# Optimization experiments

Measured on AMD Instinct MI355X. Metric: run time of the kernel, lower is better.

Reference implementation:

```python
import jax, jax.numpy as jnp
import numpy as np
from jax import lax

D_MODEL = 64      # feature_dim
D_STATE = 16      # state_dim
D_CONV = 4        # conv_dim
EXPAND = 2
D_INNER = EXPAND * D_MODEL          # 128
DT_RANK = (D_MODEL + 15) // 16      # ceil(d_model/16) = 4, mamba default
IN_DIM = 64
LN_EPS = 1e-3                        # keras LayerNormalization default epsilon


def setup_inputs() -> dict:
    key = jax.random.key(0)
    ks = jax.random.split(key, 12)
    B, L = 16, 8192
    s = 0.02
    x = jax.random.normal(ks[0], (B, L, IN_DIM), jnp.float32)
    W_in = jax.random.normal(ks[1], (IN_DIM, D_MODEL), jnp.float32) * s
    b_in = jnp.zeros((D_MODEL,), jnp.float32)
    in_proj_w = jax.random.normal(ks[2], (D_MODEL, 2 * D_INNER), jnp.float32) * s
    conv_w = jax.random.normal(ks[3], (D_INNER, D_CONV), jnp.float32) * 0.1
    conv_b = jnp.zeros((D_INNER,), jnp.float32)
    x_proj_w = jax.random.normal(ks[4], (D_INNER, DT_RANK + 2 * D_STATE), jnp.float32) * s
    dt_proj_w = jax.random.normal(ks[5], (DT_RANK, D_INNER), jnp.float32) * (DT_RANK ** -0.5)
    # dt bias init so softplus(dt) lands roughly in [dt_min, dt_max]
    dt = jnp.exp(jax.random.uniform(ks[6], (D_INNER,)) * (np.log(0.1) - np.log(0.001)) + np.log(0.001))
    dt_proj_b = dt + jnp.log(-jnp.expm1(-dt))  # inverse softplus
    A_log = jnp.log(jnp.broadcast_to(jnp.arange(1, D_STATE + 1, dtype=jnp.float32), (D_INNER, D_STATE)))
    D_skip = jnp.ones((D_INNER,), jnp.float32)
    out_proj_w = jax.random.normal(ks[7], (D_INNER, D_MODEL), jnp.float32) * s
    ln_gamma = jnp.ones((D_MODEL,), jnp.float32)
    ln_beta = jnp.zeros((D_MODEL,), jnp.float32)
    return {"x": x, "W_in": W_in, "b_in": b_in, "in_proj_w": in_proj_w,
            "conv_w": conv_w, "conv_b": conv_b, "x_proj_w": x_proj_w,
            "dt_proj_w": dt_proj_w, "dt_proj_b": dt_proj_b, "A_log": A_log,
            "D_skip": D_skip, "out_proj_w": out_proj_w,
            "ln_gamma": ln_gamma, "ln_beta": ln_beta}


def reference(x, W_in, b_in, in_proj_w, conv_w, conv_b, x_proj_w,
              dt_proj_w, dt_proj_b, A_log, D_skip, out_proj_w, ln_gamma, ln_beta):
    B, L, _ = x.shape
    # Conv1D kernel_size=1 input projection
    xin = x @ W_in + b_in                          # [B,L,D_MODEL]
    # --- Mamba ---
    xz = xin @ in_proj_w                           # [B,L,2*D_INNER]
    xc, z = xz[..., :D_INNER], xz[..., D_INNER:]
    # causal depthwise conv (groups=d_inner, padding=d_conv-1, crop to L)
    xp = jnp.pad(xc, ((0, 0), (D_CONV - 1, 0), (0, 0)))
    xconv = conv_b
    for k in range(D_CONV):
        xconv = xconv + xp[:, k:k + L, :] * conv_w[:, k]
    u = jax.nn.silu(xconv)                         # [B,L,D_INNER]
    dbc = u @ x_proj_w                             # [B,L,DT_RANK+2*D_STATE]
    dt = jax.nn.softplus(dbc[..., :DT_RANK] @ dt_proj_w + dt_proj_b)   # [B,L,D_INNER]
    Bm = dbc[..., DT_RANK:DT_RANK + D_STATE]       # [B,L,D_STATE]
    Cm = dbc[..., DT_RANK + D_STATE:]              # [B,L,D_STATE]
    A = -jnp.exp(A_log)                            # [D_INNER,D_STATE]

    def step(h, xs):
        dt_t, b_t, c_t, u_t = xs                   # [B,Di],[B,Ds],[B,Ds],[B,Di]
        dA = jnp.exp(dt_t[:, :, None] * A)         # [B,Di,Ds]
        h = dA * h + (dt_t * u_t)[:, :, None] * b_t[:, None, :]
        y = jnp.einsum('bds,bs->bd', h, c_t)
        return h, y

    xs = (jnp.swapaxes(dt, 0, 1), jnp.swapaxes(Bm, 0, 1),
          jnp.swapaxes(Cm, 0, 1), jnp.swapaxes(u, 0, 1))
    h0 = jnp.zeros((B, D_INNER, D_STATE), x.dtype)
    _, ys = lax.scan(step, h0, xs)                 # ys: [L,B,D_INNER]
    y = jnp.swapaxes(ys, 0, 1) + u * D_skip
    y = y * jax.nn.silu(z)
    h_out = y @ out_proj_w                         # [B,L,D_MODEL]
    # residual + LayerNorm
    res = h_out + xin
    mu = jnp.mean(res, axis=-1, keepdims=True)
    var = jnp.mean(jnp.square(res - mu), axis=-1, keepdims=True)
    return ln_gamma * (res - mu) * lax.rsqrt(var + LN_EPS) + ln_beta
```

## Files before the change

kernel.cpp:

```cpp
#include <hip/hip_runtime.h>
#include <hip/hip_bf16.h>

#define B_SZ   16
#define L_SZ   8192
#define DM     64
#define DI     128
#define NCH    128
#define CLEN   64
#define CH     64
#define RT     80
#define PA     72
#define PU     136
#define PC     132
#define LN_EPS 1e-3f

typedef float  f4 __attribute__((ext_vector_type(4)));
typedef short  s8 __attribute__((ext_vector_type(8)));
typedef unsigned short u16;
typedef unsigned int   u32;
#define MFMA16 __builtin_amdgcn_mfma_f32_16x16x32_bf16

__device__ __forceinline__ u16 f2bfu(float f) {
    u32 u = __float_as_uint(f);
    return (u16)((u + 0x7FFFu + ((u >> 16) & 1u)) >> 16);
}
__device__ __forceinline__ u32 pk2bf(float a, float b) {
    return (u32)f2bfu(a) | ((u32)f2bfu(b) << 16);
}
__device__ __forceinline__ float bflo(u32 u) { return __uint_as_float(u << 16); }
__device__ __forceinline__ float bfhi(u32 u) { return __uint_as_float(u & 0xFFFF0000u); }
__device__ __forceinline__ float bfu2f(u16 h) { return __uint_as_float((u32)h << 16); }
__device__ __forceinline__ float fsig(float v) {
    return __builtin_amdgcn_rcpf(1.f + __expf(-v));
}
__device__ __forceinline__ float fsp(float v) {
    return fmaxf(v, 0.f) + __logf(1.f + __expf(-fabsf(v)));
}

__global__ __launch_bounds__(256) void k_prep(
    const float* __restrict__ W_in, const float* __restrict__ in_proj,
    const float* __restrict__ x_proj, const float* __restrict__ Wout,
    u16* __restrict__ Wf1, u16* __restrict__ Wf2,
    u16* __restrict__ Wf3, u16* __restrict__ Wf4)
{
    const int tid = threadIdx.x;
    for (int g = tid; g < 512; g += 256) {
        int lane = g & 63, ks = (g >> 6) & 1, nt = g >> 7;
        int n = nt * 16 + (lane & 15), kb = ks * 32 + (lane >> 4) * 8;
        for (int j = 0; j < 8; j++) Wf1[g * 8 + j] = f2bfu(W_in[(kb + j) * 64 + n]);
    }
    for (int g = tid; g < 2048; g += 256) {
        int lane = g & 63, ks = (g >> 6) & 1, nt = g >> 7;
        int n = nt * 16 + (lane & 15), kb = ks * 32 + (lane >> 4) * 8;
        for (int j = 0; j < 8; j++) Wf2[g * 8 + j] = f2bfu(in_proj[(kb + j) * 256 + n]);
    }
    for (int g = tid; g < 768; g += 256) {
        int lane = g & 63, ks = (g >> 6) & 3, nt = g >> 8;
        int n = nt * 16 + (lane & 15), kb = ks * 32 + (lane >> 4) * 8;
        for (int j = 0; j < 8; j++)
            Wf3[g * 8 + j] = f2bfu(n < 36 ? x_proj[(kb + j) * 36 + n] : 0.f);
    }
    for (int g = tid; g < 1024; g += 256) {
        int lane = g & 63, ks = (g >> 6) & 3, nt = g >> 8;
        int n = nt * 16 + (lane & 15), kb = ks * 32 + (lane >> 4) * 8;
        for (int j = 0; j < 8; j++) Wf4[g * 8 + j] = f2bfu(Wout[(kb + j) * 64 + n]);
    }
}

__global__ __launch_bounds__(256) void k_frontend(
    const float* __restrict__ x, const float* __restrict__ b_in,
    const float* __restrict__ conv_w, const float* __restrict__ conv_b,
    const float* __restrict__ dt_w, const float* __restrict__ dt_b,
    const u16* __restrict__ Wf1, const u16* __restrict__ Wf2, const u16* __restrict__ Wf3,
    float* __restrict__ xin_g, u16* __restrict__ u_g, float* __restrict__ dt_g,
    float* __restrict__ B_g, float* __restrict__ C_g, u16* __restrict__ sz_g)
{
    __shared__ __align__(16) char sm[41088];
    u16*   smA   = (u16*)sm;
    u16*   smB   = (u16*)(sm + 11520);
    u16*   smU   = (u16*)sm;
    float* smDtr = (float*)(sm + 17408);
    u16*   smC   = (u16*)(sm + 23040);

    const int tid = threadIdx.x;
    const int w = tid >> 6, lane = tid & 63;
    const int n16 = lane & 15, quad = lane >> 4;
    const int b = blockIdx.y, c0 = blockIdx.x * CH;
    const long long tokbase = (long long)b * L_SZ + c0;

    for (int idx = tid; idx < RT * 16; idx += 256) {
        int r = idx >> 4, c4 = idx & 15;
        int l = c0 - 3 + r;
        float4 v = make_float4(0.f, 0.f, 0.f, 0.f);
        if (r < 67 && l >= 0)
            v = *(const float4*)(x + ((long long)b * L_SZ + l) * 64 + c4 * 4);
        *(uint2*)((char*)smA + r * 144 + c4 * 8) = make_uint2(pk2bf(v.x, v.y), pk2bf(v.z, v.w));
    }
    __syncthreads();

    {
        s8 b0 = *(const s8*)(Wf1 + ((w * 2 + 0) * 64 + lane) * 8);
        s8 b1 = *(const s8*)(Wf1 + ((w * 2 + 1) * 64 + lane) * 8);
        float bias = b_in[w * 16 + n16];
        for (int m = 0; m < 5; m++) {
            int ar = m * 16 + n16;
            s8 a0 = *(const s8*)(smA + ar * PA + quad * 8);
            s8 a1 = *(const s8*)(smA + ar * PA + 32 + quad * 8);
            f4 acc = {0.f, 0.f, 0.f, 0.f};
            acc = MFMA16(a0, b0, acc, 0, 0, 0);
            acc = MFMA16(a1, b1, acc, 0, 0, 0);
#pragma unroll
            for (int reg = 0; reg < 4; reg++) {
                int rr = m * 16 + quad * 4 + reg;
                float v = acc[reg] + bias;
                smB[rr * PA + w * 16 + n16] = f2bfu(v);
                if (rr >= 3 && rr < 67)
                    xin_g[(tokbase + rr - 3) * 64 + w * 16 + n16] = v;
            }
        }
    }
    __syncthreads();

    {
        s8 bf[4][2];
#pragma unroll
        for (int i = 0; i < 4; i++)
#pragma unroll
            for (int ks = 0; ks < 2; ks++)
                bf[i][ks] = *(const s8*)(Wf2 + (((w * 4 + i) * 2 + ks) * 64 + lane) * 8);
        for (int m = 0; m < 5; m++) {
            int ar = m * 16 + n16;
            s8 a0 = *(const s8*)(smB + ar * PA + quad * 8);
            s8 a1 = *(const s8*)(smB + ar * PA + 32 + quad * 8);
#pragma unroll
            for (int i = 0; i < 4; i++) {
                f4 acc = {0.f, 0.f, 0.f, 0.f};
                acc = MFMA16(a0, bf[i][0], acc, 0, 0, 0);
                acc = MFMA16(a1, bf[i][1], acc, 0, 0, 0);
                int cg = (w * 4 + i) * 16 + n16;
#pragma unroll
                for (int reg = 0; reg < 4; reg++) {
                    int rr = m * 16 + quad * 4 + reg;
                    float v = acc[reg];
                    if (cg < 128) {
                        if (rr < 67) {
                            int l = c0 - 3 + rr;
                            smC[rr * PC + cg] = f2bfu(l >= 0 ? v : 0.f);
                        }
                    } else if (rr >= 3 && rr < 67) {
                        sz_g[(tokbase + rr - 3) * 128 + (cg - 128)] = f2bfu(v * fsig(v));
                    }
                }
            }
        }
    }
    __syncthreads();

    {
        const int d2 = lane * 2, ctb = w * 16;
        float4 cw0 = ((const float4*)conv_w)[d2];
        float4 cw1 = ((const float4*)conv_w)[d2 + 1];
        float cb0 = conv_b[d2], cb1 = conv_b[d2 + 1];
        u32 r0 = *(const u32*)((char*)smC + (ctb + 0) * 264 + lane * 4);
        u32 r1 = *(const u32*)((char*)smC + (ctb + 1) * 264 + lane * 4);
        u32 r2 = *(const u32*)((char*)smC + (ctb + 2) * 264 + lane * 4);
#pragma unroll 4
        for (int j = 0; j < 16; j++) {
            int ct = ctb + j;
            u32 r3 = *(const u32*)((char*)smC + (ct + 3) * 264 + lane * 4);
            float v0 = cb0 + bflo(r0) * cw0.x + bflo(r1) * cw0.y + bflo(r2) * cw0.z + bflo(r3) * cw0.w;
            float v1 = cb1 + bfhi(r0) * cw1.x + bfhi(r1) * cw1.y + bfhi(r2) * cw1.z + bfhi(r3) * cw1.w;
            u32 pk = pk2bf(v0 * fsig(v0), v1 * fsig(v1));
            *(u32*)(u_g + (tokbase + ct) * 128 + d2) = pk;
            *(u32*)(smU + ct * PU + d2) = pk;
            r0 = r1; r1 = r2; r2 = r3;
        }
    }
    __syncthreads();

    {
        s8 bf3[3][4];
#pragma unroll
        for (int nt = 0; nt < 3; nt++)
#pragma unroll
            for (int ks = 0; ks < 4; ks++)
                bf3[nt][ks] = *(const s8*)(Wf3 + ((nt * 4 + ks) * 64 + lane) * 8);
        f4 acc[3] = {{0.f,0.f,0.f,0.f},{0.f,0.f,0.f,0.f},{0.f,0.f,0.f,0.f}};
        int ar = w * 16 + n16;
#pragma unroll
        for (int ks = 0; ks < 4; ks++) {
            s8 a = *(const s8*)(smU + ar * PU + ks * 32 + quad * 8);
#pragma unroll
            for (int nt = 0; nt < 3; nt++) acc[nt] = MFMA16(a, bf3[nt][ks], acc[nt], 0, 0, 0);
        }
#pragma unroll
        for (int nt = 0; nt < 3; nt++) {
            int c = nt * 16 + n16;
#pragma unroll
            for (int reg = 0; reg < 4; reg++) {
                int rr = w * 16 + quad * 4 + reg;
                float v = acc[nt][reg];
                long long t = tokbase + rr;
                if (c < 4)       smDtr[rr * 4 + c] = v;
                else if (c < 20) B_g[t * 16 + (c - 4)] = v;
                else if (c < 36) C_g[t * 16 + (c - 20)] = v;
            }
        }
    }
    __syncthreads();

    {
        const int o2 = lane * 2, grp = w;
        float w00 = dt_w[o2],       w01 = dt_w[o2 + 1];
        float w10 = dt_w[128 + o2], w11 = dt_w[128 + o2 + 1];
        float w20 = dt_w[256 + o2], w21 = dt_w[256 + o2 + 1];
        float w30 = dt_w[384 + o2], w31 = dt_w[384 + o2 + 1];
        float b0 = dt_b[o2], b1 = dt_b[o2 + 1];
#pragma unroll 4
        for (int j = 0; j < 16; j++) {
            int ct = grp * 16 + j;
            float4 q = *(const float4*)(smDtr + ct * 4);
            float v0 = b0 + q.x * w00 + q.y * w10 + q.z * w20 + q.w * w30;
            float v1 = b1 + q.x * w01 + q.y * w11 + q.z * w21 + q.w * w31;
            *(float2*)(dt_g + (tokbase + ct) * 128 + o2) = make_float2(fsp(v0), fsp(v1));
        }
    }
}

__global__ __launch_bounds__(128) void k_scan1(
    const float* __restrict__ dt_g, const u16* __restrict__ u_g,
    const float* __restrict__ B_g, const float* __restrict__ A_log,
    float* __restrict__ hl_ws, float* __restrict__ sdt_ws)
{
    const int d = threadIdx.x, c = blockIdx.x, b = blockIdx.y;
    float A[16];
#pragma unroll
    for (int s = 0; s < 16; s++) A[s] = -__expf(A_log[d * 16 + s]);
    const float A0 = A[0];
    bool chain = true;
#pragma unroll
    for (int s = 1; s < 16; s++)
        chain = chain && (fabsf(A[s] - (float)(s + 1) * A0) <= 1e-4f * fabsf(A[s]));

    float h[16];
#pragma unroll
    for (int s = 0; s < 16; s++) h[s] = 0.f;
    float sdt = 0.f;
    const long long tok0 = (long long)b * L_SZ + (long long)c * CLEN;

    if (chain) {
        for (int i = 0; i < CLEN; i++) {
            const long long t = tok0 + i;
            float dtv = dt_g[t * 128 + d];
            float uv  = bfu2f(u_g[t * 128 + d]);
            const float4* Bp = (const float4*)(B_g + t * 16);
            float4 B0 = Bp[0], B1 = Bp[1], B2 = Bp[2], B3 = Bp[3];
            float Bv[16] = { B0.x, B0.y, B0.z, B0.w, B1.x, B1.y, B1.z, B1.w,
                             B2.x, B2.y, B2.z, B2.w, B3.x, B3.y, B3.z, B3.w };
            float du = dtv * uv;  sdt += dtv;
            float p = __expf(dtv * A0), dA = p;
            h[0] = dA * h[0] + du * Bv[0];
#pragma unroll
            for (int s = 1; s < 16; s++) { dA *= p; h[s] = dA * h[s] + du * Bv[s]; }
        }
    } else {
        for (int i = 0; i < CLEN; i++) {
            const long long t = tok0 + i;
            float dtv = dt_g[t * 128 + d];
            float uv  = bfu2f(u_g[t * 128 + d]);
            const float4* Bp = (const float4*)(B_g + t * 16);
            float4 B0 = Bp[0], B1 = Bp[1], B2 = Bp[2], B3 = Bp[3];
            float Bv[16] = { B0.x, B0.y, B0.z, B0.w, B1.x, B1.y, B1.z, B1.w,
                             B2.x, B2.y, B2.z, B2.w, B3.x, B3.y, B3.z, B3.w };
            float du = dtv * uv;  sdt += dtv;
#pragma unroll
            for (int s = 0; s < 16; s++) h[s] = __expf(dtv * A[s]) * h[s] + du * Bv[s];
        }
    }

    float4* hp4 = (float4*)(hl_ws + (((long long)b * NCH + c) * 128 + d) * 16);
    hp4[0] = make_float4(h[0], h[1], h[2], h[3]);
    hp4[1] = make_float4(h[4], h[5], h[6], h[7]);
    hp4[2] = make_float4(h[8], h[9], h[10], h[11]);
    hp4[3] = make_float4(h[12], h[13], h[14], h[15]);
    sdt_ws[((long long)b * NCH + c) * 128 + d] = sdt;
}

__global__ __launch_bounds__(256) void k_combine(
    const float* __restrict__ A_log, const float* __restrict__ hl_ws,
    const float* __restrict__ sdt_ws, float* __restrict__ hin_ws)
{
    int gid = blockIdx.x * 256 + threadIdx.x;
    int b = gid >> 11;
    int rem = gid & 2047;
    int d = rem >> 4;
    float A = -__expf(A_log[rem]);
    float h = 0.f;
    for (int c = 0; c < NCH; c++) {
        long long o = ((long long)b * NCH + c) * 2048 + rem;
        hin_ws[o] = h;
        float sdt = sdt_ws[((long long)b * NCH + c) * 128 + d];
        h = __expf(A * sdt) * h + hl_ws[o];
    }
}

__global__ __launch_bounds__(128) void k_scan3(
    const float* __restrict__ dt_g, const u16* __restrict__ u_g,
    const float* __restrict__ B_g, const float* __restrict__ C_g,
    const u16* __restrict__ sz_g, const float* __restrict__ A_log,
    const float* __restrict__ D_skip, const float* __restrict__ hin_ws,
    u16* __restrict__ y_g)
{
    const int d = threadIdx.x, c = blockIdx.x, b = blockIdx.y;
    float A[16];
#pragma unroll
    for (int s = 0; s < 16; s++) A[s] = -__expf(A_log[d * 16 + s]);
    const float A0 = A[0];
    bool chain = true;
#pragma unroll
    for (int s = 1; s < 16; s++)
        chain = chain && (fabsf(A[s] - (float)(s + 1) * A0) <= 1e-4f * fabsf(A[s]));

    float h[16];
    {
        const float4* hp = (const float4*)(hin_ws + (((long long)b * NCH + c) * 128 + d) * 16);
        float4 h0 = hp[0], h1 = hp[1], h2 = hp[2], h3 = hp[3];
        h[0]=h0.x; h[1]=h0.y; h[2]=h0.z; h[3]=h0.w;
        h[4]=h1.x; h[5]=h1.y; h[6]=h1.z; h[7]=h1.w;
        h[8]=h2.x; h[9]=h2.y; h[10]=h2.z; h[11]=h2.w;
        h[12]=h3.x; h[13]=h3.y; h[14]=h3.z; h[15]=h3.w;
    }
    const float Dv = D_skip[d];
    const long long tok0 = (long long)b * L_SZ + (long long)c * CLEN;

    if (chain) {
        for (int i = 0; i < CLEN; i++) {
            const long long t = tok0 + i;
            float dtv = dt_g[t * 128 + d];
            float uv  = bfu2f(u_g[t * 128 + d]);
            const float4* Bp = (const float4*)(B_g + t * 16);
            float4 B0 = Bp[0], B1 = Bp[1], B2 = Bp[2], B3 = Bp[3];
            float Bv[16] = { B0.x, B0.y, B0.z, B0.w, B1.x, B1.y, B1.z, B1.w,
                             B2.x, B2.y, B2.z, B2.w, B3.x, B3.y, B3.z, B3.w };
            const float4* Cp = (const float4*)(C_g + t * 16);
            float4 C0 = Cp[0], C1 = Cp[1], C2 = Cp[2], C3 = Cp[3];
            float Cv[16] = { C0.x, C0.y, C0.z, C0.w, C1.x, C1.y, C1.z, C1.w,
                             C2.x, C2.y, C2.z, C2.w, C3.x, C3.y, C3.z, C3.w };
            float du = dtv * uv;
            float p = __expf(dtv * A0), dA = p;
            h[0] = dA * h[0] + du * Bv[0];
            float ysum = h[0] * Cv[0];
#pragma unroll
            for (int s = 1; s < 16; s++) {
                dA *= p;
                h[s] = dA * h[s] + du * Bv[s];
                ysum += h[s] * Cv[s];
            }
            float szv = bfu2f(sz_g[t * 128 + d]);
            y_g[t * 128 + d] = f2bfu((ysum + uv * Dv) * szv);
        }
    } else {
        for (int i = 0; i < CLEN; i++) {
            const long long t = tok0 + i;
            float dtv = dt_g[t * 128 + d];
            float uv  = bfu2f(u_g[t * 128 + d]);
            const float4* Bp = (const float4*)(B_g + t * 16);
            float4 B0 = Bp[0], B1 = Bp[1], B2 = Bp[2], B3 = Bp[3];
            float Bv[16] = { B0.x, B0.y, B0.z, B0.w, B1.x, B1.y, B1.z, B1.w,
                             B2.x, B2.y, B2.z, B2.w, B3.x, B3.y, B3.z, B3.w };
            const float4* Cp = (const float4*)(C_g + t * 16);
            float4 C0 = Cp[0], C1 = Cp[1], C2 = Cp[2], C3 = Cp[3];
            float Cv[16] = { C0.x, C0.y, C0.z, C0.w, C1.x, C1.y, C1.z, C1.w,
                             C2.x, C2.y, C2.z, C2.w, C3.x, C3.y, C3.z, C3.w };
            float du = dtv * uv;
            float ysum = 0.f;
#pragma unroll
            for (int s = 0; s < 16; s++) {
                h[s] = __expf(dtv * A[s]) * h[s] + du * Bv[s];
                ysum += h[s] * Cv[s];
            }
            float szv = bfu2f(sz_g[t * 128 + d]);
            y_g[t * 128 + d] = f2bfu((ysum + uv * Dv) * szv);
        }
    }
}

__global__ __launch_bounds__(256) void k_epilogue(
    const u16* __restrict__ y_g, const float* __restrict__ xin_g,
    const u16* __restrict__ Wf4, const float* __restrict__ gamma,
    const float* __restrict__ beta, float* __restrict__ out)
{
    __shared__ __align__(16) char sm[34048];
    u16*   yA  = (u16*)sm;
    float* smR = (float*)(sm + 17408);

    const int tid = threadIdx.x;
    const int w = tid >> 6, lane = tid & 63;
    const int n16 = lane & 15, quad = lane >> 4;
    const long long t0 = (long long)blockIdx.x * 64;

    for (int idx = tid; idx < 64 * 64; idx += 256) {
        int r = idx >> 6, cp = idx & 63;
        u32 v = ((const u32*)y_g)[(t0 + r) * 64 + cp];
        *(u32*)((char*)yA + r * 272 + cp * 4) = v;
    }
    __syncthreads();

    {
        s8 bf[4];
#pragma unroll
        for (int ks = 0; ks < 4; ks++)
            bf[ks] = *(const s8*)(Wf4 + ((w * 4 + ks) * 64 + lane) * 8);
#pragma unroll
        for (int m = 0; m < 4; m++) {
            int ar = m * 16 + n16;
            f4 acc = {0.f, 0.f, 0.f, 0.f};
#pragma unroll
            for (int ks = 0; ks < 4; ks++) {
                s8 a = *(const s8*)(yA + ar * PU + ks * 32 + quad * 8);
                acc = MFMA16(a, bf[ks], acc, 0, 0, 0);
            }
#pragma unroll
            for (int reg = 0; reg < 4; reg++) {
                int rr = m * 16 + quad * 4 + reg;
                smR[rr * 65 + w * 16 + n16] = acc[reg];
            }
        }
    }
    __syncthreads();

    {
        int o = tid & 63, wv = tid >> 6;
        float g = gamma[o], bb = beta[o];
        for (int j = 0; j < 16; j++) {
            int rr = wv * 16 + j;
            float r = smR[rr * 65 + o] + xin_g[(t0 + rr) * 64 + o];
            float s = r;
#pragma unroll
            for (int mS = 0; mS < 6; mS++) s += __shfl_xor(s, 1 << mS, 64);
            float mu = s * (1.f / 64.f);
            float dv = r - mu;
            float vs = dv * dv;
#pragma unroll
            for (int mS = 0; mS < 6; mS++) vs += __shfl_xor(vs, 1 << mS, 64);
            out[(t0 + rr) * 64 + o] = g * dv * rsqrtf(vs * (1.f / 64.f) + LN_EPS) + bb;
        }
    }
}

extern "C" void kernel_launch(void* const* d_in, const int* in_sizes, int n_in,
                              void* d_out, int out_size, void* d_ws, size_t ws_size,
                              hipStream_t stream)
{
    const float* x       = (const float*)d_in[0];
    const float* W_in    = (const float*)d_in[1];
    const float* b_in    = (const float*)d_in[2];
    const float* in_proj = (const float*)d_in[3];
    const float* conv_w  = (const float*)d_in[4];
    const float* conv_b  = (const float*)d_in[5];
    const float* x_proj  = (const float*)d_in[6];
    const float* dt_w    = (const float*)d_in[7];
    const float* dt_b    = (const float*)d_in[8];
    const float* A_log   = (const float*)d_in[9];
    const float* D_skip  = (const float*)d_in[10];
    const float* Wout    = (const float*)d_in[11];
    const float* gamma   = (const float*)d_in[12];
    const float* beta    = (const float*)d_in[13];
    float* out = (float*)d_out;

    const long long NT = (long long)B_SZ * L_SZ;
    char* ws = (char*)d_ws;
    float*  xin_g = (float*)ws;   ws += NT * 64 * 4;
    float*  dt_g  = (float*)ws;   ws += NT * 128 * 4;
    float*  B_g   = (float*)ws;   ws += NT * 16 * 4;
    float*  C_g   = (float*)ws;   ws += NT * 16 * 4;
    u16*    u_g   = (u16*)ws;     ws += NT * 128 * 2;
    u16*    sz_g  = (u16*)ws;     ws += NT * 128 * 2;
    u16*    y_g   = (u16*)ws;     ws += NT * 128 * 2;
    float*  hl_ws  = (float*)ws;  ws += (long long)B_SZ * NCH * 2048 * 4;
    float*  sdt_ws = (float*)ws;  ws += (long long)B_SZ * NCH * 128 * 4;
    float*  hin_ws = (float*)ws;  ws += (long long)B_SZ * NCH * 2048 * 4;
    u16* Wf1 = (u16*)ws; ws += 4096 * 2;
    u16* Wf2 = (u16*)ws; ws += 16384 * 2;
    u16* Wf3 = (u16*)ws; ws += 6144 * 2;
    u16* Wf4 = (u16*)ws; ws += 8192 * 2;

    k_prep<<<1, 256, 0, stream>>>(W_in, in_proj, x_proj, Wout, Wf1, Wf2, Wf3, Wf4);

    k_frontend<<<dim3(L_SZ / CH, B_SZ), 256, 0, stream>>>(
        x, b_in, conv_w, conv_b, dt_w, dt_b, Wf1, Wf2, Wf3,
        xin_g, u_g, dt_g, B_g, C_g, sz_g);

    k_scan1<<<dim3(NCH, B_SZ), 128, 0, stream>>>(
        dt_g, u_g, B_g, A_log, hl_ws, sdt_ws);

    k_combine<<<128, 256, 0, stream>>>(A_log, hl_ws, sdt_ws, hin_ws);

    k_scan3<<<dim3(NCH, B_SZ), 128, 0, stream>>>(
        dt_g, u_g, B_g, C_g, sz_g, A_log, D_skip, hin_ws, y_g);

    k_epilogue<<<2048, 256, 0, stream>>>(y_g, xin_g, Wf4, gamma, beta, out);
}
```

Measured before the change: 310.4 us.

## Fuse chunk-local scan into frontend and fuse output scan with epilogue

The first chunked scan pass moves into the frontend kernel and reads dt inputs, u and B from shared memory, recomputing dt from the low-rank projection, with state split across two thread halves. The second scan pass is merged with the out-projection and LayerNorm epilogue, so y stays in shared memory and the y_g round trip and two launches go away. In exchange, only half the threads do scan work in the fused output kernel, the frontend gains more shared memory and a serial tail, and occupancy may drop.

```diff
diff --git a/kernel.cpp b/kernel.cpp
--- a/kernel.cpp
+++ b/kernel.cpp
@@ -71,16 +71,19 @@
     const float* __restrict__ x, const float* __restrict__ b_in,
     const float* __restrict__ conv_w, const float* __restrict__ conv_b,
     const float* __restrict__ dt_w, const float* __restrict__ dt_b,
+    const float* __restrict__ A_log,
     const u16* __restrict__ Wf1, const u16* __restrict__ Wf2, const u16* __restrict__ Wf3,
     float* __restrict__ xin_g, u16* __restrict__ u_g, float* __restrict__ dt_g,
-    float* __restrict__ B_g, float* __restrict__ C_g, u16* __restrict__ sz_g)
+    float* __restrict__ B_g, float* __restrict__ C_g, u16* __restrict__ sz_g,
+    float* __restrict__ hl_ws, float* __restrict__ sdt_ws)
 {
-    __shared__ __align__(16) char sm[41088];
+    __shared__ __align__(16) char sm[45184];
     u16*   smA   = (u16*)sm;
     u16*   smB   = (u16*)(sm + 11520);
     u16*   smU   = (u16*)sm;
     float* smDtr = (float*)(sm + 17408);
     u16*   smC   = (u16*)(sm + 23040);
+    float* smBB  = (float*)(sm + 41088);
 
     const int tid = threadIdx.x;
     const int w = tid >> 6, lane = tid & 63;
@@ -202,7 +205,7 @@
                 float v = acc[nt][reg];
                 long long t = tokbase + rr;
                 if (c < 4)       smDtr[rr * 4 + c] = v;
-                else if (c < 20) B_g[t * 16 + (c - 4)] = v;
+                else if (c < 20) { B_g[t * 16 + (c - 4)] = v; smBB[rr * 16 + (c - 4)] = v; }
                 else if (c < 36) C_g[t * 16 + (c - 20)] = v;
             }
         }
@@ -225,65 +228,61 @@
             *(float2*)(dt_g + (tokbase + ct) * 128 + o2) = make_float2(fsp(v0), fsp(v1));
         }
     }
-}
-
-__global__ __launch_bounds__(128) void k_scan1(
-    const float* __restrict__ dt_g, const u16* __restrict__ u_g,
-    const float* __restrict__ B_g, const float* __restrict__ A_log,
-    float* __restrict__ hl_ws, float* __restrict__ sdt_ws)
-{
-    const int d = threadIdx.x, c = blockIdx.x, b = blockIdx.y;
-    float A[16];
-#pragma unroll
-    for (int s = 0; s < 16; s++) A[s] = -__expf(A_log[d * 16 + s]);
-    const float A0 = A[0];
-    bool chain = true;
-#pragma unroll
-    for (int s = 1; s < 16; s++)
-        chain = chain && (fabsf(A[s] - (float)(s + 1) * A0) <= 1e-4f * fabsf(A[s]));
-
-    float h[16];
-#pragma unroll
-    for (int s = 0; s < 16; s++) h[s] = 0.f;
-    float sdt = 0.f;
-    const long long tok0 = (long long)b * L_SZ + (long long)c * CLEN;
-
-    if (chain) {
-        for (int i = 0; i < CLEN; i++) {
-            const long long t = tok0 + i;
-            float dtv = dt_g[t * 128 + d];
-            float uv  = bfu2f(u_g[t * 128 + d]);
-            const float4* Bp = (const float4*)(B_g + t * 16);
-            float4 B0 = Bp[0], B1 = Bp[1], B2 = Bp[2], B3 = Bp[3];
-            float Bv[16] = { B0.x, B0.y, B0.z, B0.w, B1.x, B1.y, B1.z, B1.w,
-                             B2.x, B2.y, B2.z, B2.w, B3.x, B3.y, B3.z, B3.w };
-            float du = dtv * uv;  sdt += dtv;
-            float p = __expf(dtv * A0), dA = p;
-            h[0] = dA * h[0] + du * Bv[0];
-#pragma unroll
-            for (int s = 1; s < 16; s++) { dA *= p; h[s] = dA * h[s] + du * Bv[s]; }
-        }
-    } else {
-        for (int i = 0; i < CLEN; i++) {
-            const long long t = tok0 + i;
-            float dtv = dt_g[t * 128 + d];
-            float uv  = bfu2f(u_g[t * 128 + d]);
-            const float4* Bp = (const float4*)(B_g + t * 16);
-            float4 B0 = Bp[0], B1 = Bp[1], B2 = Bp[2], B3 = Bp[3];
-            float Bv[16] = { B0.x, B0.y, B0.z, B0.w, B1.x, B1.y, B1.z, B1.w,
-                             B2.x, B2.y, B2.z, B2.w, B3.x, B3.y, B3.z, B3.w };
-            float du = dtv * uv;  sdt += dtv;
-#pragma unroll
-            for (int s = 0; s < 16; s++) h[s] = __expf(dtv * A[s]) * h[s] + du * Bv[s];
-        }
-    }
-
-    float4* hp4 = (float4*)(hl_ws + (((long long)b * NCH + c) * 128 + d) * 16);
-    hp4[0] = make_float4(h[0], h[1], h[2], h[3]);
-    hp4[1] = make_float4(h[4], h[5], h[6], h[7]);
-    hp4[2] = make_float4(h[8], h[9], h[10], h[11]);
-    hp4[3] = make_float4(h[12], h[13], h[14], h[15]);
-    sdt_ws[((long long)b * NCH + c) * 128 + d] = sdt;
+
+    {
+        const int d = tid & 127, oct = tid >> 7;
+        const float bw0 = dt_w[d], bw1 = dt_w[128 + d], bw2 = dt_w[256 + d], bw3 = dt_w[384 + d];
+        const float bdt = dt_b[d];
+        const float A0 = -__expf(A_log[d * 16]);
+        float Aq[8];
+#pragma unroll
+        for (int k = 0; k < 8; k++) Aq[k] = -__expf(A_log[d * 16 + oct * 8 + k]);
+        bool chain = true;
+#pragma unroll
+        for (int k = 0; k < 8; k++)
+            chain = chain && (fabsf(Aq[k] - (float)(oct * 8 + k + 1) * A0) <= 1e-4f * fabsf(Aq[k]));
+
+        float h[8];
+#pragma unroll
+        for (int k = 0; k < 8; k++) h[k] = 0.f;
+        float sdt = 0.f;
+
+        if (chain) {
+            for (int i = 0; i < CH; i++) {
+                float4 q = *(const float4*)(smDtr + i * 4);
+                float dtv = fsp(bdt + q.x * bw0 + q.y * bw1 + q.z * bw2 + q.w * bw3);
+                float uv = bfu2f(smU[i * PU + d]);
+                float du = dtv * uv;  sdt += dtv;
+                float4 b0 = *(const float4*)(smBB + i * 16 + oct * 8);
+                float4 b1 = *(const float4*)(smBB + i * 16 + oct * 8 + 4);
+                float Bv[8] = {b0.x, b0.y, b0.z, b0.w, b1.x, b1.y, b1.z, b1.w};
+                float p = __expf(dtv * A0);
+                float dA;
+                if (oct == 0) dA = p;
+                else { float p2 = p * p, p4 = p2 * p2, p8 = p4 * p4; dA = p8 * p; }
+                h[0] = dA * h[0] + du * Bv[0];
+#pragma unroll
+                for (int k = 1; k < 8; k++) { dA *= p; h[k] = dA * h[k] + du * Bv[k]; }
+            }
+        } else {
+            for (int i = 0; i < CH; i++) {
+                float4 q = *(const float4*)(smDtr + i * 4);
+                float dtv = fsp(bdt + q.x * bw0 + q.y * bw1 + q.z * bw2 + q.w * bw3);
+                float uv = bfu2f(smU[i * PU + d]);
+                float du = dtv * uv;  sdt += dtv;
+                float4 b0 = *(const float4*)(smBB + i * 16 + oct * 8);
+                float4 b1 = *(const float4*)(smBB + i * 16 + oct * 8 + 4);
+                float Bv[8] = {b0.x, b0.y, b0.z, b0.w, b1.x, b1.y, b1.z, b1.w};
+#pragma unroll
+                for (int k = 0; k < 8; k++) h[k] = __expf(dtv * Aq[k]) * h[k] + du * Bv[k];
+            }
+        }
+        float4* hp = (float4*)(hl_ws + (((long long)b * NCH + blockIdx.x) * 128 + d) * 16 + oct * 8);
+        hp[0] = make_float4(h[0], h[1], h[2], h[3]);
+        hp[1] = make_float4(h[4], h[5], h[6], h[7]);
+        if (oct == 0)
+            sdt_ws[((long long)b * NCH + blockIdx.x) * 128 + d] = sdt;
+    }
 }
 
 __global__ __launch_bounds__(256) void k_combine(
@@ -304,108 +303,101 @@
     }
 }
 
-__global__ __launch_bounds__(128) void k_scan3(
+__global__ __launch_bounds__(256) void k_scan3f(
     const float* __restrict__ dt_g, const u16* __restrict__ u_g,
     const float* __restrict__ B_g, const float* __restrict__ C_g,
     const u16* __restrict__ sz_g, const float* __restrict__ A_log,
     const float* __restrict__ D_skip, const float* __restrict__ hin_ws,
-    u16* __restrict__ y_g)
+    const u16* __restrict__ Wf4, const float* __restrict__ xin_g,
+    const float* __restrict__ gamma, const float* __restrict__ beta,
+    float* __restrict__ out)
 {
-    const int d = threadIdx.x, c = blockIdx.x, b = blockIdx.y;
-    float A[16];
-#pragma unroll
-    for (int s = 0; s < 16; s++) A[s] = -__expf(A_log[d * 16 + s]);
-    const float A0 = A[0];
-    bool chain = true;
-#pragma unroll
-    for (int s = 1; s < 16; s++)
-        chain = chain && (fabsf(A[s] - (float)(s + 1) * A0) <= 1e-4f * fabsf(A[s]));
-
-    float h[16];
-    {
-        const float4* hp = (const float4*)(hin_ws + (((long long)b * NCH + c) * 128 + d) * 16);
-        float4 h0 = hp[0], h1 = hp[1], h2 = hp[2], h3 = hp[3];
-        h[0]=h0.x; h[1]=h0.y; h[2]=h0.z; h[3]=h0.w;
-        h[4]=h1.x; h[5]=h1.y; h[6]=h1.z; h[7]=h1.w;
-        h[8]=h2.x; h[9]=h2.y; h[10]=h2.z; h[11]=h2.w;
-        h[12]=h3.x; h[13]=h3.y; h[14]=h3.z; h[15]=h3.w;
-    }
-    const float Dv = D_skip[d];
-    const long long tok0 = (long long)b * L_SZ + (long long)c * CLEN;
-
-    if (chain) {
-        for (int i = 0; i < CLEN; i++) {
-            const long long t = tok0 + i;
-            float dtv = dt_g[t * 128 + d];
-            float uv  = bfu2f(u_g[t * 128 + d]);
-            const float4* Bp = (const float4*)(B_g + t * 16);
-            float4 B0 = Bp[0], B1 = Bp[1], B2 = Bp[2], B3 = Bp[3];
-            float Bv[16] = { B0.x, B0.y, B0.z, B0.w, B1.x, B1.y, B1.z, B1.w,
-                             B2.x, B2.y, B2.z, B2.w, B3.x, B3.y, B3.z, B3.w };
-            const float4* Cp = (const float4*)(C_g + t * 16);
-            float4 C0 = Cp[0], C1 = Cp[1], C2 = Cp[2], C3 = Cp[3];
-            float Cv[16] = { C0.x, C0.y, C0.z, C0.w, C1.x, C1.y, C1.z, C1.w,
-                             C2.x, C2.y, C2.z, C2.w, C3.x, C3.y, C3.z, C3.w };
-            float du = dtv * uv;
-            float p = __expf(dtv * A0), dA = p;
-            h[0] = dA * h[0] + du * Bv[0];
-            float ysum = h[0] * Cv[0];
-#pragma unroll
-            for (int s = 1; s < 16; s++) {
-                dA *= p;
-                h[s] = dA * h[s] + du * Bv[s];
-                ysum += h[s] * Cv[s];
-            }
-            float szv = bfu2f(sz_g[t * 128 + d]);
-            y_g[t * 128 + d] = f2bfu((ysum + uv * Dv) * szv);
-        }
-    } else {
-        for (int i = 0; i < CLEN; i++) {
-            const long long t = tok0 + i;
-            float dtv = dt_g[t * 128 + d];
-            float uv  = bfu2f(u_g[t * 128 + d]);
-            const float4* Bp = (const float4*)(B_g + t * 16);
-            float4 B0 = Bp[0], B1 = Bp[1], B2 = Bp[2], B3 = Bp[3];
-            float Bv[16] = { B0.x, B0.y, B0.z, B0.w, B1.x, B1.y, B1.z, B1.w,
-                             B2.x, B2.y, B2.z, B2.w, B3.x, B3.y, B3.z, B3.w };
-            const float4* Cp = (const float4*)(C_g + t * 16);
-            float4 C0 = Cp[0], C1 = Cp[1], C2 = Cp[2], C3 = Cp[3];
-            float Cv[16] = { C0.x, C0.y, C0.z, C0.w, C1.x, C1.y, C1.z, C1.w,
-                             C2.x, C2.y, C2.z, C2.w, C3.x, C3.y, C3.z, C3.w };
-            float du = dtv * uv;
-            float ysum = 0.f;
-#pragma unroll
-            for (int s = 0; s < 16; s++) {
-                h[s] = __expf(dtv * A[s]) * h[s] + du * Bv[s];
-                ysum += h[s] * Cv[s];
-            }
-            float szv = bfu2f(sz_g[t * 128 + d]);
-            y_g[t * 128 + d] = f2bfu((ysum + uv * Dv) * szv);
-        }
-    }
-}
-
-__global__ __launch_bounds__(256) void k_epilogue(
-    const u16* __restrict__ y_g, const float* __restrict__ xin_g,
-    const u16* __restrict__ Wf4, const float* __restrict__ gamma,
-    const float* __restrict__ beta, float* __restrict__ out)
-{
-    __shared__ __align__(16) char sm[34048];
-    u16*   yA  = (u16*)sm;
-    float* smR = (float*)(sm + 17408);
+    __shared__ __align__(16) char sm[17408];
+    u16*   smY = (u16*)sm;
+    float* smR = (float*)sm;
 
     const int tid = threadIdx.x;
+    const int c = blockIdx.x, b = blockIdx.y;
+    const long long t0 = (long long)b * L_SZ + (long long)c * CLEN;
+
+    if (tid < 128) {
+        const int d = tid;
+        float A[16];
+#pragma unroll
+        for (int s = 0; s < 16; s++) A[s] = -__expf(A_log[d * 16 + s]);
+        const float A0 = A[0];
+        bool chain = true;
+#pragma unroll
+        for (int s = 1; s < 16; s++)
+            chain = chain && (fabsf(A[s] - (float)(s + 1) * A0) <= 1e-4f * fabsf(A[s]));
+
+        float h[16];
+        {
+            const float4* hp = (const float4*)(hin_ws + (((long long)b * NCH + c) * 128 + d) * 16);
+            float4 h0 = hp[0], h1 = hp[1], h2 = hp[2], h3 = hp[3];
+            h[0]=h0.x; h[1]=h0.y; h[2]=h0.z; h[3]=h0.w;
+            h[4]=h1.x; h[5]=h1.y; h[6]=h1.z; h[7]=h1.w;
+            h[8]=h2.x; h[9]=h2.y; h[10]=h2.z; h[11]=h2.w;
+            h[12]=h3.x; h[13]=h3.y; h[14]=h3.z; h[15]=h3.w;
+        }
+        const float Dv = D_skip[d];
+
+        if (chain) {
+            for (int i = 0; i < CLEN; i++) {
+                const long long t = t0 + i;
+                float dtv = dt_g[t * 128 + d];
+                float uv  = bfu2f(u_g[t * 128 + d]);
+                const float4* Bp = (const float4*)(B_g + t * 16);
+                float4 B0 = Bp[0], B1 = Bp[1], B2 = Bp[2], B3 = Bp[3];
+                float Bv[16] = { B0.x, B0.y, B0.z, B0.w, B1.x, B1.y, B1.z, B1.w,
+                                 B2.x, B2.y, B2.z, B2.w, B3.x, B3.y, B3.z, B3.w };
+                const float4* Cp = (const float4*)(C_g + t * 16);
+                float4 C0 = Cp[0], C1 = Cp[1], C2 = Cp[2], C3 = Cp[3];
+                float Cv[16] = { C0.x, C0.y, C0.z, C0.w, C1.x, C1.y, C1.z, C1.w,
+                                 C2.x, C2.y, C2.z, C2.w, C3.x, C3.y, C3.z, C3.w };
+                float du = dtv * uv;
+                float p = __expf(dtv * A0), dA = p;
+                h[0] = dA * h[0] + du * Bv[0];
+                float ysum = h[0] * Cv[0];
+#pragma unroll
+                for (int s = 1; s < 16; s++) {
+                    dA *= p;
+                    h[s] = dA * h[s] + du * Bv[s];
+                    ysum += h[s] * Cv[s];
+                }
+                float szv = bfu2f(sz_g[t * 128 + d]);
+                smY[i * PU + d] = f2bfu((ysum + uv * Dv) * szv);
+            }
+        } else {
+            for (int i = 0; i < CLEN; i++) {
+                const long long t = t0 + i;
+                float dtv = dt_g[t * 128 + d];
+                float uv  = bfu2f(u_g[t * 128 + d]);
+                const float4* Bp = (const float4*)(B_g + t * 16);
+                float4 B0 = Bp[0], B1 = Bp[1], B2 = Bp[2], B3 = Bp[3];
+                float Bv[16] = { B0.x, B0.y, B0.z, B0.w, B1.x, B1.y, B1.z, B1.w,
+                                 B2.x, B2.y, B2.z, B2.w, B3.x, B3.y, B3.z, B3.w };
+                const float4* Cp = (const float4*)(C_g + t * 16);
+                float4 C0 = Cp[0], C1 = Cp[1], C2 = Cp[2], C3 = Cp[3];
+                float Cv[16] = { C0.x, C0.y, C0.z, C0.w, C1.x, C1.y, C1.z, C1.w,
+                                 C2.x, C2.y, C2.z, C2.w, C3.x, C3.y, C3.z, C3.w };
+                float du = dtv * uv;
+                float ysum = 0.f;
+#pragma unroll
+                for (int s = 0; s < 16; s++) {
+                    h[s] = __expf(dtv * A[s]) * h[s] + du * Bv[s];
+                    ysum += h[s] * Cv[s];
+                }
+                float szv = bfu2f(sz_g[t * 128 + d]);
+                smY[i * PU + d] = f2bfu((ysum + uv * Dv) * szv);
+            }
+        }
+    }
+    __syncthreads();
+
     const int w = tid >> 6, lane = tid & 63;
     const int n16 = lane & 15, quad = lane >> 4;
-    const long long t0 = (long long)blockIdx.x * 64;
-
-    for (int idx = tid; idx < 64 * 64; idx += 256) {
-        int r = idx >> 6, cp = idx & 63;
-        u32 v = ((const u32*)y_g)[(t0 + r) * 64 + cp];
-        *(u32*)((char*)yA + r * 272 + cp * 4) = v;
-    }
-    __syncthreads();
-
+    f4 accs[4];
     {
         s8 bf[4];
 #pragma unroll
@@ -417,16 +409,21 @@
             f4 acc = {0.f, 0.f, 0.f, 0.f};
 #pragma unroll
             for (int ks = 0; ks < 4; ks++) {
-                s8 a = *(const s8*)(yA + ar * PU + ks * 32 + quad * 8);
+                s8 a = *(const s8*)(smY + ar * PU + ks * 32 + quad * 8);
                 acc = MFMA16(a, bf[ks], acc, 0, 0, 0);
             }
-#pragma unroll
-            for (int reg = 0; reg < 4; reg++) {
-                int rr = m * 16 + quad * 4 + reg;
-                smR[rr * 65 + w * 16 + n16] = acc[reg];
-            }
-        }
-    }
+            accs[m] = acc;
+        }
+    }
+    __syncthreads();
+
+#pragma unroll
+    for (int m = 0; m < 4; m++)
+#pragma unroll
+        for (int reg = 0; reg < 4; reg++) {
+            int rr = m * 16 + quad * 4 + reg;
+            smR[rr * 65 + w * 16 + n16] = accs[m][reg];
+        }
     __syncthreads();
 
     {
@@ -476,7 +473,6 @@
     float*  C_g   = (float*)ws;   ws += NT * 16 * 4;
     u16*    u_g   = (u16*)ws;     ws += NT * 128 * 2;
     u16*    sz_g  = (u16*)ws;     ws += NT * 128 * 2;
-    u16*    y_g   = (u16*)ws;     ws += NT * 128 * 2;
     float*  hl_ws  = (float*)ws;  ws += (long long)B_SZ * NCH * 2048 * 4;
     float*  sdt_ws = (float*)ws;  ws += (long long)B_SZ * NCH * 128 * 4;
     float*  hin_ws = (float*)ws;  ws += (long long)B_SZ * NCH * 2048 * 4;
@@ -488,16 +484,12 @@
     k_prep<<<1, 256, 0, stream>>>(W_in, in_proj, x_proj, Wout, Wf1, Wf2, Wf3, Wf4);
 
     k_frontend<<<dim3(L_SZ / CH, B_SZ), 256, 0, stream>>>(
-        x, b_in, conv_w, conv_b, dt_w, dt_b, Wf1, Wf2, Wf3,
-        xin_g, u_g, dt_g, B_g, C_g, sz_g);
-
-    k_scan1<<<dim3(NCH, B_SZ), 128, 0, stream>>>(
-        dt_g, u_g, B_g, A_log, hl_ws, sdt_ws);
+        x, b_in, conv_w, conv_b, dt_w, dt_b, A_log, Wf1, Wf2, Wf3,
+        xin_g, u_g, dt_g, B_g, C_g, sz_g, hl_ws, sdt_ws);
 
     k_combine<<<128, 256, 0, stream>>>(A_log, hl_ws, sdt_ws, hin_ws);
 
-    k_scan3<<<dim3(NCH, B_SZ), 128, 0, stream>>>(
-        dt_g, u_g, B_g, C_g, sz_g, A_log, D_skip, hin_ws, y_g);
-
-    k_epilogue<<<2048, 256, 0, stream>>>(y_g, xin_g, Wf4, gamma, beta, out);
-}
+    k_scan3f<<<dim3(NCH, B_SZ), 256, 0, stream>>>(
+        dt_g, u_g, B_g, C_g, sz_g, A_log, D_skip, hin_ws, Wf4, xin_g,
+        gamma, beta, out);
+}
```

Result: slower. 318.4 us (+2.6%).

## Recompute dt in scan kernels, stage B/C in LDS, parallelize chunk combine

Applied to the files above, without the earlier changes.

The frontend no longer expands dt to the full 128 channels. It now writes only the 4-wide dt_rank projection, and both scan kernels recompute softplus(dt_proj) per token from that. This removes writing and twice re-reading a large fp32 dt buffer, at the cost of extra FMAs and a softplus in the serial scan loops. The scan kernels also stage each chunk's B and C vectors in shared memory instead of issuing per-token global loads. The combine kernel splits the 128 chunks into 4 segments per state element, merged with shuffles, which quadruples its thread count to use more of the GPU.

```diff
diff --git a/kernel.cpp b/kernel.cpp
--- a/kernel.cpp
+++ b/kernel.cpp
@@ -70,9 +70,8 @@
 __global__ __launch_bounds__(256) void k_frontend(
     const float* __restrict__ x, const float* __restrict__ b_in,
     const float* __restrict__ conv_w, const float* __restrict__ conv_b,
-    const float* __restrict__ dt_w, const float* __restrict__ dt_b,
     const u16* __restrict__ Wf1, const u16* __restrict__ Wf2, const u16* __restrict__ Wf3,
-    float* __restrict__ xin_g, u16* __restrict__ u_g, float* __restrict__ dt_g,
+    float* __restrict__ xin_g, u16* __restrict__ u_g, float* __restrict__ dtr_g,
     float* __restrict__ B_g, float* __restrict__ C_g, u16* __restrict__ sz_g)
 {
     __shared__ __align__(16) char sm[41088];
@@ -209,30 +208,34 @@
     }
     __syncthreads();
 
-    {
-        const int o2 = lane * 2, grp = w;
-        float w00 = dt_w[o2],       w01 = dt_w[o2 + 1];
-        float w10 = dt_w[128 + o2], w11 = dt_w[128 + o2 + 1];
-        float w20 = dt_w[256 + o2], w21 = dt_w[256 + o2 + 1];
-        float w30 = dt_w[384 + o2], w31 = dt_w[384 + o2 + 1];
-        float b0 = dt_b[o2], b1 = dt_b[o2 + 1];
-#pragma unroll 4
-        for (int j = 0; j < 16; j++) {
-            int ct = grp * 16 + j;
-            float4 q = *(const float4*)(smDtr + ct * 4);
-            float v0 = b0 + q.x * w00 + q.y * w10 + q.z * w20 + q.w * w30;
-            float v1 = b1 + q.x * w01 + q.y * w11 + q.z * w21 + q.w * w31;
-            *(float2*)(dt_g + (tokbase + ct) * 128 + o2) = make_float2(fsp(v0), fsp(v1));
-        }
-    }
+    if (tid < 64)
+        *(float4*)(dtr_g + (tokbase + tid) * 4) = *(const float4*)(smDtr + tid * 4);
 }
 
 __global__ __launch_bounds__(128) void k_scan1(
-    const float* __restrict__ dt_g, const u16* __restrict__ u_g,
+    const float* __restrict__ dtr_g, const u16* __restrict__ u_g,
     const float* __restrict__ B_g, const float* __restrict__ A_log,
+    const float* __restrict__ dt_w, const float* __restrict__ dt_b,
     float* __restrict__ hl_ws, float* __restrict__ sdt_ws)
 {
+    __shared__ __align__(16) float smQ[CLEN * 4];
+    __shared__ __align__(16) float smBs[CLEN * 16];
+
     const int d = threadIdx.x, c = blockIdx.x, b = blockIdx.y;
+    const long long tok0 = (long long)b * L_SZ + (long long)c * CLEN;
+
+    {
+        const float4* srcB = (const float4*)(B_g + tok0 * 16);
+        float4* dstB = (float4*)smBs;
+        dstB[d] = srcB[d];
+        dstB[d + 128] = srcB[d + 128];
+        if (d < 64) ((float4*)smQ)[d] = ((const float4*)(dtr_g + tok0 * 4))[d];
+    }
+    __syncthreads();
+
+    const float w0 = dt_w[d], w1 = dt_w[128 + d], w2 = dt_w[256 + d], w3 = dt_w[384 + d];
+    const float bdt = dt_b[d];
+
     float A[16];
 #pragma unroll
     for (int s = 0; s < 16; s++) A[s] = -__expf(A_log[d * 16 + s]);
@@ -246,17 +249,18 @@
 #pragma unroll
     for (int s = 0; s < 16; s++) h[s] = 0.f;
     float sdt = 0.f;
-    const long long tok0 = (long long)b * L_SZ + (long long)c * CLEN;
 
     if (chain) {
         for (int i = 0; i < CLEN; i++) {
-            const long long t = tok0 + i;
-            float dtv = dt_g[t * 128 + d];
-            float uv  = bfu2f(u_g[t * 128 + d]);
-            const float4* Bp = (const float4*)(B_g + t * 16);
-            float4 B0 = Bp[0], B1 = Bp[1], B2 = Bp[2], B3 = Bp[3];
-            float Bv[16] = { B0.x, B0.y, B0.z, B0.w, B1.x, B1.y, B1.z, B1.w,
-                             B2.x, B2.y, B2.z, B2.w, B3.x, B3.y, B3.z, B3.w };
+            float4 q = *(const float4*)(smQ + i * 4);
+            float dtv = fsp(bdt + q.x * w0 + q.y * w1 + q.z * w2 + q.w * w3);
+            float uv  = bfu2f(u_g[(tok0 + i) * 128 + d]);
+            float4 b0 = *(const float4*)(smBs + i * 16);
+            float4 b1 = *(const float4*)(smBs + i * 16 + 4);
+            float4 b2 = *(const float4*)(smBs + i * 16 + 8);
+            float4 b3 = *(const float4*)(smBs + i * 16 + 12);
+            float Bv[16] = { b0.x, b0.y, b0.z, b0.w, b1.x, b1.y, b1.z, b1.w,
+                             b2.x, b2.y, b2.z, b2.w, b3.x, b3.y, b3.z, b3.w };
             float du = dtv * uv;  sdt += dtv;
             float p = __expf(dtv * A0), dA = p;
             h[0] = dA * h[0] + du * Bv[0];
@@ -265,13 +269,15 @@
         }
     } else {
         for (int i = 0; i < CLEN; i++) {
-            const long long t = tok0 + i;
-            float dtv = dt_g[t * 128 + d];
-            float uv  = bfu2f(u_g[t * 128 + d]);
-            const float4* Bp = (const float4*)(B_g + t * 16);
-            float4 B0 = Bp[0], B1 = Bp[1], B2 = Bp[2], B3 = Bp[3];
-            float Bv[16] = { B0.x, B0.y, B0.z, B0.w, B1.x, B1.y, B1.z, B1.w,
-                             B2.x, B2.y, B2.z, B2.w, B3.x, B3.y, B3.z, B3.w };
+            float4 q = *(const float4*)(smQ + i * 4);
+            float dtv = fsp(bdt + q.x * w0 + q.y * w1 + q.z * w2 + q.w * w3);
+            float uv  = bfu2f(u_g[(tok0 + i) * 128 + d]);
+            float4 b0 = *(const float4*)(smBs + i * 16);
+            float4 b1 = *(const float4*)(smBs + i * 16 + 4);
+            float4 b2 = *(const float4*)(smBs + i * 16 + 8);
+            float4 b3 = *(const float4*)(smBs + i * 16 + 12);
+            float Bv[16] = { b0.x, b0.y, b0.z, b0.w, b1.x, b1.y, b1.z, b1.w,
+                             b2.x, b2.y, b2.z, b2.w, b3.x, b3.y, b3.z, b3.w };
             float du = dtv * uv;  sdt += dtv;
 #pragma unroll
             for (int s = 0; s < 16; s++) h[s] = __expf(dtv * A[s]) * h[s] + du * Bv[s];
@@ -290,28 +296,70 @@
     const float* __restrict__ A_log, const float* __restrict__ hl_ws,
     const float* __restrict__ sdt_ws, float* __restrict__ hin_ws)
 {
-    int gid = blockIdx.x * 256 + threadIdx.x;
-    int b = gid >> 11;
-    int rem = gid & 2047;
-    int d = rem >> 4;
-    float A = -__expf(A_log[rem]);
-    float h = 0.f;
-    for (int c = 0; c < NCH; c++) {
-        long long o = ((long long)b * NCH + c) * 2048 + rem;
-        hin_ws[o] = h;
-        float sdt = sdt_ws[((long long)b * NCH + c) * 128 + d];
-        h = __expf(A * sdt) * h + hl_ws[o];
+    const int tid = threadIdx.x, lane = tid & 63;
+    const int seg = tid & 3;
+    const int sIdx = blockIdx.x * 64 + (tid >> 2);
+    const int b = sIdx >> 11, rem = sIdx & 2047, d = rem >> 4;
+    const float A = -__expf(A_log[rem]);
+    const int cBeg = seg * 32;
+    const long long hlBase  = ((long long)b * NCH) * 2048 + rem;
+    const long long sdtBase = ((long long)b * NCH) * 128 + d;
+
+    float hloc = 0.f, ssum = 0.f;
+#pragma unroll 4
+    for (int c = cBeg; c < cBeg + 32; c++) {
+        float sd = sdt_ws[sdtBase + (long long)c * 128];
+        ssum += sd;
+        hloc = __expf(A * sd) * hloc + hl_ws[hlBase + (long long)c * 2048];
+    }
+
+    float H = 0.f;
+    const int gbase = lane & ~3;
+#pragma unroll
+    for (int k = 0; k < 3; k++) {
+        float hs = __shfl(hloc, gbase + k, 64);
+        float ss = __shfl(ssum, gbase + k, 64);
+        if (k < seg) H = hs + H * __expf(A * ss);
+    }
+
+    float h = H;
+#pragma unroll 4
+    for (int c = cBeg; c < cBeg + 32; c++) {
+        hin_ws[hlBase + (long long)c * 2048] = h;
+        float sd = sdt_ws[sdtBase + (long long)c * 128];
+        h = __expf(A * sd) * h + hl_ws[hlBase + (long long)c * 2048];
     }
 }
 
 __global__ __launch_bounds__(128) void k_scan3(
-    const float* __restrict__ dt_g, const u16* __restrict__ u_g,
+    const float* __restrict__ dtr_g, const u16* __restrict__ u_g,
     const float* __restrict__ B_g, const float* __restrict__ C_g,
     const u16* __restrict__ sz_g, const float* __restrict__ A_log,
+    const float* __restrict__ dt_w, const float* __restrict__ dt_b,
     const float* __restrict__ D_skip, const float* __restrict__ hin_ws,
     u16* __restrict__ y_g)
 {
+    __shared__ __align__(16) float smQ[CLEN * 4];
+    __shared__ __align__(16) float smBs[CLEN * 16];
+    __shared__ __align__(16) float smCs[CLEN * 16];
+
     const int d = threadIdx.x, c = blockIdx.x, b = blockIdx.y;
+    const long long tok0 = (long long)b * L_SZ + (long long)c * CLEN;
+
+    {
+        const float4* srcB = (const float4*)(B_g + tok0 * 16);
+        const float4* srcC = (const float4*)(C_g + tok0 * 16);
+        ((float4*)smBs)[d] = srcB[d];
+        ((float4*)smBs)[d + 128] = srcB[d + 128];
+        ((float4*)smCs)[d] = srcC[d];
+        ((float4*)smCs)[d + 128] = srcC[d + 128];
+        if (d < 64) ((float4*)smQ)[d] = ((const float4*)(dtr_g + tok0 * 4))[d];
+    }
+    __syncthreads();
+
+    const float w0 = dt_w[d], w1 = dt_w[128 + d], w2 = dt_w[256 + d], w3 = dt_w[384 + d];
+    const float bdt = dt_b[d];
+
     float A[16];
 #pragma unroll
     for (int s = 0; s < 16; s++) A[s] = -__expf(A_log[d * 16 + s]);
@@ -331,21 +379,24 @@
         h[12]=h3.x; h[13]=h3.y; h[14]=h3.z; h[15]=h3.w;
     }
     const float Dv = D_skip[d];
-    const long long tok0 = (long long)b * L_SZ + (long long)c * CLEN;
 
     if (chain) {
         for (int i = 0; i < CLEN; i++) {
-            const long long t = tok0 + i;
-            float dtv = dt_g[t * 128 + d];
-            float uv  = bfu2f(u_g[t * 128 + d]);
-            const float4* Bp = (const float4*)(B_g + t * 16);
-            float4 B0 = Bp[0], B1 = Bp[1], B2 = Bp[2], B3 = Bp[3];
-            float Bv[16] = { B0.x, B0.y, B0.z, B0.w, B1.x, B1.y, B1.z, B1.w,
-                             B2.x, B2.y, B2.z, B2.w, B3.x, B3.y, B3.z, B3.w };
-            const float4* Cp = (const float4*)(C_g + t * 16);
-            float4 C0 = Cp[0], C1 = Cp[1], C2 = Cp[2], C3 = Cp[3];
-            float Cv[16] = { C0.x, C0.y, C0.z, C0.w, C1.x, C1.y, C1.z, C1.w,
-                             C2.x, C2.y, C2.z, C2.w, C3.x, C3.y, C3.z, C3.w };
+            float4 q = *(const float4*)(smQ + i * 4);
+            float dtv = fsp(bdt + q.x * w0 + q.y * w1 + q.z * w2 + q.w * w3);
+            float uv  = bfu2f(u_g[(tok0 + i) * 128 + d]);
+            float4 b0 = *(const float4*)(smBs + i * 16);
+            float4 b1 = *(const float4*)(smBs + i * 16 + 4);
+            float4 b2 = *(const float4*)(smBs + i * 16 + 8);
+            float4 b3 = *(const float4*)(smBs + i * 16 + 12);
+            float Bv[16] = { b0.x, b0.y, b0.z, b0.w, b1.x, b1.y, b1.z, b1.w,
+                             b2.x, b2.y, b2.z, b2.w, b3.x, b3.y, b3.z, b3.w };
+            float4 c0v = *(const float4*)(smCs + i * 16);
+            float4 c1v = *(const float4*)(smCs + i * 16 + 4);
+            float4 c2v = *(const float4*)(smCs + i * 16 + 8);
+            float4 c3v = *(const float4*)(smCs + i * 16 + 12);
+            float Cv[16] = { c0v.x, c0v.y, c0v.z, c0v.w, c1v.x, c1v.y, c1v.z, c1v.w,
+                             c2v.x, c2v.y, c2v.z, c2v.w, c3v.x, c3v.y, c3v.z, c3v.w };
             float du = dtv * uv;
             float p = __expf(dtv * A0), dA = p;
             h[0] = dA * h[0] + du * Bv[0];
@@ -356,22 +407,26 @@
                 h[s] = dA * h[s] + du * Bv[s];
                 ysum += h[s] * Cv[s];
             }
-            float szv = bfu2f(sz_g[t * 128 + d]);
-            y_g[t * 128 + d] = f2bfu((ysum + uv * Dv) * szv);
+            float szv = bfu2f(sz_g[(tok0 + i) * 128 + d]);
+            y_g[(tok0 + i) * 128 + d] = f2bfu((ysum + uv * Dv) * szv);
         }
     } else {
         for (int i = 0; i < CLEN; i++) {
-            const long long t = tok0 + i;
-            float dtv = dt_g[t * 128 + d];
-            float uv  = bfu2f(u_g[t * 128 + d]);
-            const float4* Bp = (const float4*)(B_g + t * 16);
-            float4 B0 = Bp[0], B1 = Bp[1], B2 = Bp[2], B3 = Bp[3];
-            float Bv[16] = { B0.x, B0.y, B0.z, B0.w, B1.x, B1.y, B1.z, B1.w,
-                             B2.x, B2.y, B2.z, B2.w, B3.x, B3.y, B3.z, B3.w };
-            const float4* Cp = (const float4*)(C_g + t * 16);
-            float4 C0 = Cp[0], C1 = Cp[1], C2 = Cp[2], C3 = Cp[3];
-            float Cv[16] = { C0.x, C0.y, C0.z, C0.w, C1.x, C1.y, C1.z, C1.w,
-                             C2.x, C2.y, C2.z, C2.w, C3.x, C3.y, C3.z, C3.w };
+            float4 q = *(const float4*)(smQ + i * 4);
+            float dtv = fsp(bdt + q.x * w0 + q.y * w1 + q.z * w2 + q.w * w3);
+            float uv  = bfu2f(u_g[(tok0 + i) * 128 + d]);
+            float4 b0 = *(const float4*)(smBs + i * 16);
+            float4 b1 = *(const float4*)(smBs + i * 16 + 4);
+            float4 b2 = *(const float4*)(smBs + i * 16 + 8);
+            float4 b3 = *(const float4*)(smBs + i * 16 + 12);
+            float Bv[16] = { b0.x, b0.y, b0.z, b0.w, b1.x, b1.y, b1.z, b1.w,
+                             b2.x, b2.y, b2.z, b2.w, b3.x, b3.y, b3.z, b3.w };
+            float4 c0v = *(const float4*)(smCs + i * 16);
+            float4 c1v = *(const float4*)(smCs + i * 16 + 4);
+            float4 c2v = *(const float4*)(smCs + i * 16 + 8);
+            float4 c3v = *(const float4*)(smCs + i * 16 + 12);
+            float Cv[16] = { c0v.x, c0v.y, c0v.z, c0v.w, c1v.x, c1v.y, c1v.z, c1v.w,
+                             c2v.x, c2v.y, c2v.z, c2v.w, c3v.x, c3v.y, c3v.z, c3v.w };
             float du = dtv * uv;
             float ysum = 0.f;
 #pragma unroll
@@ -379,8 +434,8 @@
                 h[s] = __expf(dtv * A[s]) * h[s] + du * Bv[s];
                 ysum += h[s] * Cv[s];
             }
-            float szv = bfu2f(sz_g[t * 128 + d]);
-            y_g[t * 128 + d] = f2bfu((ysum + uv * Dv) * szv);
+            float szv = bfu2f(sz_g[(tok0 + i) * 128 + d]);
+            y_g[(tok0 + i) * 128 + d] = f2bfu((ysum + uv * Dv) * szv);
         }
     }
 }
@@ -471,7 +526,7 @@
     const long long NT = (long long)B_SZ * L_SZ;
     char* ws = (char*)d_ws;
     float*  xin_g = (float*)ws;   ws += NT * 64 * 4;
-    float*  dt_g  = (float*)ws;   ws += NT * 128 * 4;
+    float*  dtr_g = (float*)ws;   ws += NT * 4 * 4;
     float*  B_g   = (float*)ws;   ws += NT * 16 * 4;
     float*  C_g   = (float*)ws;   ws += NT * 16 * 4;
     u16*    u_g   = (u16*)ws;     ws += NT * 128 * 2;
@@ -488,16 +543,16 @@
     k_prep<<<1, 256, 0, stream>>>(W_in, in_proj, x_proj, Wout, Wf1, Wf2, Wf3, Wf4);
 
     k_frontend<<<dim3(L_SZ / CH, B_SZ), 256, 0, stream>>>(
-        x, b_in, conv_w, conv_b, dt_w, dt_b, Wf1, Wf2, Wf3,
-        xin_g, u_g, dt_g, B_g, C_g, sz_g);
+        x, b_in, conv_w, conv_b, Wf1, Wf2, Wf3,
+        xin_g, u_g, dtr_g, B_g, C_g, sz_g);
 
     k_scan1<<<dim3(NCH, B_SZ), 128, 0, stream>>>(
-        dt_g, u_g, B_g, A_log, hl_ws, sdt_ws);
-
-    k_combine<<<128, 256, 0, stream>>>(A_log, hl_ws, sdt_ws, hin_ws);
+        dtr_g, u_g, B_g, A_log, dt_w, dt_b, hl_ws, sdt_ws);
+
+    k_combine<<<512, 256, 0, stream>>>(A_log, hl_ws, sdt_ws, hin_ws);
 
     k_scan3<<<dim3(NCH, B_SZ), 128, 0, stream>>>(
-        dt_g, u_g, B_g, C_g, sz_g, A_log, D_skip, hin_ws, y_g);
+        dtr_g, u_g, B_g, C_g, sz_g, A_log, dt_w, dt_b, D_skip, hin_ws, y_g);
 
     k_epilogue<<<2048, 256, 0, stream>>>(y_g, xin_g, Wf4, gamma, beta, out);
 }
```

Measured after the change: 315.6 us. Within noise of the previous version (+1.7%).
